# Kernel tuning notes

Hardware: AMD Instinct MI355X
Metric: run time of the kernel (lower is better)

## Reference

```python
import jax, jax.numpy as jnp
import numpy as np

EMBED_DIM = 1024
NUM_HEADS = 16
HEAD_DIM = EMBED_DIM // NUM_HEADS
B, T = 2, 2048


def setup_inputs() -> dict:
    key = jax.random.key(0)
    ks = jax.random.split(key, 5)
    s_in = 1.0 / np.sqrt(EMBED_DIM)
    return {
        "x": jax.random.normal(ks[0], (B, T, EMBED_DIM), dtype=jnp.float32),
        "qkv_w": jax.random.uniform(ks[1], (3 * EMBED_DIM, EMBED_DIM), jnp.float32, -s_in, s_in),
        "qkv_b": jax.random.uniform(ks[2], (3 * EMBED_DIM,), jnp.float32, -s_in, s_in),
        "out_w": jax.random.uniform(ks[3], (EMBED_DIM, EMBED_DIM), jnp.float32, -s_in, s_in),
        "out_b": jax.random.uniform(ks[4], (EMBED_DIM,), jnp.float32, -s_in, s_in),
    }


def reference(x, qkv_w, qkv_b, out_w, out_b):
    b, t, d = x.shape
    scale = HEAD_DIM ** -0.5
    # fused qkv projection: (B, T, 3D)
    qkv = jnp.einsum("btd,ed->bte", x, qkv_w) + qkv_b
    qkv = qkv.reshape(b, t, 3, NUM_HEADS, HEAD_DIM)
    q, k, v = jnp.moveaxis(qkv, 2, 0)  # each (B, T, H, Dh)
    # scores: (B, H, T, T)
    scores = jnp.einsum("bqhd,bkhd->bhqk", q, k) * scale
    attn = jax.nn.softmax(scores, axis=-1)
    # attention output: (B, T, H, Dh) -> (B, T, D)
    ctx = jnp.einsum("bhqk,bkhd->bqhd", attn, v).reshape(b, t, d)
    return jnp.einsum("btd,ed->bte", ctx, out_w) + out_b
```

## Files before the change

kernel.cpp:

```cpp
#include <hip/hip_runtime.h>

typedef __bf16 bf16;
typedef __bf16 bf16x4 __attribute__((ext_vector_type(4)));
typedef __bf16 bf16x8 __attribute__((ext_vector_type(8)));
typedef float f32x4 __attribute__((ext_vector_type(4)));

#define MFMA16(a, b, c) __builtin_amdgcn_mfma_f32_16x16x32_bf16(a, b, c, 0, 0, 0)

__device__ __forceinline__ void lds_load16(void* lds, const void* g) {
  __builtin_amdgcn_global_load_lds(
      (const __attribute__((address_space(1))) unsigned int*)g,
      (__attribute__((address_space(3))) unsigned int*)lds, 16, 0, 0);
}

__global__ void cvt3(const float* __restrict__ x, const float* __restrict__ qw,
                     const float* __restrict__ ow, bf16* __restrict__ xb,
                     bf16* __restrict__ qwb, bf16* __restrict__ owb) {
  const int i = blockIdx.x * blockDim.x + threadIdx.x;
  const float* src;
  bf16* dst;
  int k;
  if (i < 1048576) {
    src = x; dst = xb; k = i;
  } else if (i < 1048576 + 786432) {
    src = qw; dst = qwb; k = i - 1048576;
  } else {
    src = ow; dst = owb; k = i - (1048576 + 786432);
  }
  const float4 v = ((const float4*)src)[k];
  bf16x4 o;
  o[0] = (bf16)v.x; o[1] = (bf16)v.y; o[2] = (bf16)v.z; o[3] = (bf16)v.w;
  ((bf16x4*)dst)[k] = o;
}

__global__ __launch_bounds__(256, 2) void gemm_qkv(
    const bf16* __restrict__ A, const bf16* __restrict__ B,
    const float* __restrict__ bias, bf16* __restrict__ Qb,
    bf16* __restrict__ KF, bf16* __restrict__ VF) {
  const int K = 1024;
  __shared__ bf16 As[128][64];
  __shared__ bf16 Bs[128][64];
  const int tid = threadIdx.x;
  const int w = tid >> 6, lane = tid & 63;
  const int l15 = lane & 15, quad = lane >> 4;
  const int lr = lane >> 3;
  const int lc = (lane & 7) * 8;
  const int bn = blockIdx.x, bm = blockIdx.y;
  const int wm = (w >> 1) * 64, wn = (w & 1) * 64;

  const bf16* Abase = A + (size_t)(bm * 128) * K;
  const bf16* Bbase = B + (size_t)(bn * 128) * K;

  f32x4 acc[4][4] = {};

  for (int k0 = 0; k0 < K; k0 += 64) {
#pragma unroll
    for (int c = 0; c < 4; ++c) {
      const int row = w * 32 + c * 8;
      lds_load16(&As[row][0], Abase + (size_t)(row + lr) * K + k0 + lc);
      lds_load16(&Bs[row][0], Bbase + (size_t)(row + lr) * K + k0 + lc);
    }
    __syncthreads();
#pragma unroll
    for (int kk = 0; kk < 64; kk += 32) {
      bf16x8 am[4], bnf[4];
#pragma unroll
      for (int i = 0; i < 4; ++i)
        am[i] = *(const bf16x8*)&As[wm + i * 16 + l15][kk + quad * 8];
#pragma unroll
      for (int j = 0; j < 4; ++j)
        bnf[j] = *(const bf16x8*)&Bs[wn + j * 16 + l15][kk + quad * 8];
#pragma unroll
      for (int i = 0; i < 4; ++i)
#pragma unroll
        for (int j = 0; j < 4; ++j)
          acc[i][j] = MFMA16(am[i], bnf[j], acc[i][j]);
    }
    __syncthreads();
  }

#pragma unroll
  for (int j = 0; j < 4; ++j) {
    const int gcol = bn * 128 + wn + j * 16 + l15;
    const float bv = bias[gcol];
#pragma unroll
    for (int i = 0; i < 4; ++i) {
      const int t0 = bm * 128 + wm + i * 16 + quad * 4;
      if (gcol < 1024) {
#pragma unroll
        for (int r = 0; r < 4; ++r)
          Qb[(size_t)(t0 + r) * 1024 + gcol] =
              (bf16)((acc[i][j][r] + bv) * 0.18033688f);
      } else if (gcol < 2048) {
        const int dhl = gcol - 1024;
        const int hh = dhl >> 6, dh = dhl & 63;
        const int tl = t0 & 2047, bb = t0 >> 11;
        const size_t frag = ((size_t)(bb * 16 + hh) * 32 + (tl >> 6)) * 8 +
                            ((tl & 63) >> 4) * 2 + (dh >> 5);
        bf16* p = &KF[frag * 512 +
                      (size_t)(((dh >> 3) & 3) * 16 + (tl & 15)) * 8 + (dh & 7)];
#pragma unroll
        for (int r = 0; r < 4; ++r) p[r * 8] = (bf16)(acc[i][j][r] + bv);
      } else {
        const int dhl = gcol - 2048;
        const int hh = dhl >> 6, dh = dhl & 63;
        const int tl = t0 & 2047, bb = t0 >> 11;
        const size_t frag = ((size_t)(bb * 16 + hh) * 32 + (tl >> 6)) * 8 +
                            (dh >> 4) * 2 + ((tl & 63) >> 5);
        bf16x4 pv;
#pragma unroll
        for (int r = 0; r < 4; ++r) pv[r] = (bf16)(acc[i][j][r] + bv);
        *(bf16x4*)&VF[frag * 512 +
                      (size_t)(((tl & 31) >> 3) * 16 + (dh & 15)) * 8 +
                      (tl & 7)] = pv;
      }
    }
  }
}

__global__ __launch_bounds__(256, 2) void gemm_out(
    const bf16* __restrict__ A, const bf16* __restrict__ B,
    const float* __restrict__ bias, float* __restrict__ Cf) {
  __shared__ bf16 As[64][64];
  __shared__ bf16 Bs[128][64];
  const int tid = threadIdx.x;
  const int w = tid >> 6, lane = tid & 63;
  const int l15 = lane & 15, quad = lane >> 4;
  const int lr = lane >> 3, lc = (lane & 7) * 8;
  const int bn = blockIdx.x, bm = blockIdx.y;

  const bf16* Abase = A + (size_t)(bm * 64) * 1024;
  const bf16* Bbase = B + (size_t)(bn * 128) * 1024;

  f32x4 acc[4][2] = {};

  for (int k0 = 0; k0 < 1024; k0 += 64) {
#pragma unroll
    for (int c = 0; c < 2; ++c) {
      const int row = w * 16 + c * 8;
      lds_load16(&As[row][0], Abase + (size_t)(row + lr) * 1024 + k0 + lc);
    }
#pragma unroll
    for (int c = 0; c < 4; ++c) {
      const int row = w * 32 + c * 8;
      lds_load16(&Bs[row][0], Bbase + (size_t)(row + lr) * 1024 + k0 + lc);
    }
    __syncthreads();
#pragma unroll
    for (int kk = 0; kk < 64; kk += 32) {
      bf16x8 am[4], bnf[2];
#pragma unroll
      for (int i = 0; i < 4; ++i)
        am[i] = *(const bf16x8*)&As[i * 16 + l15][kk + quad * 8];
#pragma unroll
      for (int j = 0; j < 2; ++j)
        bnf[j] = *(const bf16x8*)&Bs[w * 32 + j * 16 + l15][kk + quad * 8];
#pragma unroll
      for (int i = 0; i < 4; ++i)
#pragma unroll
        for (int j = 0; j < 2; ++j)
          acc[i][j] = MFMA16(am[i], bnf[j], acc[i][j]);
    }
    __syncthreads();
  }

#pragma unroll
  for (int j = 0; j < 2; ++j) {
    const int gcol = bn * 128 + w * 32 + j * 16 + l15;
    const float bv = bias[gcol];
#pragma unroll
    for (int i = 0; i < 4; ++i)
#pragma unroll
      for (int r = 0; r < 4; ++r) {
        const int grow = bm * 64 + i * 16 + quad * 4 + r;
        Cf[(size_t)grow * 1024 + gcol] = acc[i][j][r] + bv;
      }
  }
}

__global__ __launch_bounds__(256, 2) void attn(const bf16* __restrict__ Qb,
                                               const bf16* __restrict__ KF,
                                               const bf16* __restrict__ VF,
                                               bf16* __restrict__ CTX) {
  __shared__ bf16 Ps[128][72];
  const int tid = threadIdx.x, w = tid >> 6, lane = tid & 63;
  const int l15 = lane & 15, quad = lane >> 4;
  const int blk = blockIdx.x;
  const int slot = blk & 7, grp = blk >> 3;
  const int qt = grp & 15, bh = (grp >> 4) * 8 + slot;
  const int h = bh & 15, b = bh >> 4;
  const int q0 = qt * 128;

  const bf16* qrow0 =
      Qb + (size_t)(b * 2048 + q0 + w * 32 + l15) * 1024 + h * 64;
  const bf16* qrow1 = qrow0 + (size_t)16 * 1024;
  const bf16x8 bq0a = *(const bf16x8*)&qrow0[quad * 8];
  const bf16x8 bq0b = *(const bf16x8*)&qrow0[32 + quad * 8];
  const bf16x8 bq1a = *(const bf16x8*)&qrow1[quad * 8];
  const bf16x8 bq1b = *(const bf16x8*)&qrow1[32 + quad * 8];

  const bf16* kfb = KF + (size_t)(b * 16 + h) * 131072 + (size_t)lane * 8;
  const bf16* vfb = VF + (size_t)(b * 16 + h) * 131072 + (size_t)lane * 8;

  bf16x8 kf[2][4], vf[2][4];
#pragma unroll
  for (int j = 0; j < 4; ++j)
#pragma unroll
    for (int k2 = 0; k2 < 2; ++k2) {
      kf[k2][j] = *(const bf16x8*)&kfb[(j * 2 + k2) << 9];
      vf[k2][j] = *(const bf16x8*)&vfb[(j * 2 + k2) << 9];
    }

  float l_run[2] = {0.f, 0.f};
  f32x4 o[2][4] = {};

  for (int kt6 = 0; kt6 < 32; ++kt6) {
    f32x4 s[2][4] = {};
#pragma unroll
    for (int k2 = 0; k2 < 2; ++k2)
#pragma unroll
      for (int j = 0; j < 4; ++j) {
        s[0][j] = MFMA16(kf[k2][j], k2 ? bq0b : bq0a, s[0][j]);
        s[1][j] = MFMA16(kf[k2][j], k2 ? bq1b : bq1a, s[1][j]);
      }

    {
      const bf16* kn = kfb + ((size_t)(kt6 + 1) << 12);
#pragma unroll
      for (int j = 0; j < 4; ++j)
#pragma unroll
        for (int k2 = 0; k2 < 2; ++k2)
          kf[k2][j] = *(const bf16x8*)&kn[(j * 2 + k2) << 9];
    }

#pragma unroll
    for (int i = 0; i < 2; ++i) {
      float sum = 0.f;
#pragma unroll
      for (int j = 0; j < 4; ++j) {
        bf16x4 pk;
#pragma unroll
        for (int r = 0; r < 4; ++r) {
          const float p = __builtin_amdgcn_exp2f(s[i][j][r]);
          sum += p;
          pk[r] = (bf16)p;
        }
        *(bf16x4*)&Ps[w * 32 + i * 16 + l15][j * 16 + quad * 4] = pk;
      }
      l_run[i] += sum;
    }

#pragma unroll
    for (int k2 = 0; k2 < 2; ++k2) {
      const bf16x8 bp0 = *(const bf16x8*)&Ps[w * 32 + l15][k2 * 32 + quad * 8];
      const bf16x8 bp1 =
          *(const bf16x8*)&Ps[w * 32 + 16 + l15][k2 * 32 + quad * 8];
#pragma unroll
      for (int j = 0; j < 4; ++j) {
        o[0][j] = MFMA16(vf[k2][j], bp0, o[0][j]);
        o[1][j] = MFMA16(vf[k2][j], bp1, o[1][j]);
      }
    }

    {
      const bf16* vn = vfb + ((size_t)(kt6 + 1) << 12);
#pragma unroll
      for (int j = 0; j < 4; ++j)
#pragma unroll
        for (int k2 = 0; k2 < 2; ++k2)
          vf[k2][j] = *(const bf16x8*)&vn[(j * 2 + k2) << 9];
    }
  }

#pragma unroll
  for (int i = 0; i < 2; ++i) {
    l_run[i] += __shfl_xor(l_run[i], 16);
    l_run[i] += __shfl_xor(l_run[i], 32);
  }

#pragma unroll
  for (int i = 0; i < 2; ++i) {
    const float inv = 1.f / l_run[i];
    bf16* crow =
        CTX + (size_t)(b * 2048 + q0 + w * 32 + i * 16 + l15) * 1024 + h * 64;
#pragma unroll
    for (int j = 0; j < 4; ++j) {
      bf16x4 ov;
#pragma unroll
      for (int r = 0; r < 4; ++r) ov[r] = (bf16)(o[i][j][r] * inv);
      *(bf16x4*)&crow[j * 16 + quad * 4] = ov;
    }
  }
}

extern "C" void kernel_launch(void* const* d_in, const int* in_sizes, int n_in,
                              void* d_out, int out_size, void* d_ws,
                              size_t ws_size, hipStream_t stream) {
  const float* x = (const float*)d_in[0];
  const float* qkv_w = (const float*)d_in[1];
  const float* qkv_b = (const float*)d_in[2];
  const float* out_w = (const float*)d_in[3];
  const float* out_b = (const float*)d_in[4];
  float* out = (float*)d_out;

  bf16* xb = (bf16*)d_ws;
  bf16* wqkv = xb + (size_t)4096 * 1024;
  bf16* wout = wqkv + (size_t)3072 * 1024;
  bf16* qb = wout + (size_t)1024 * 1024;
  bf16* kf = qb + (size_t)4096 * 1024;
  bf16* vf = kf + (size_t)4096 * 1024;
  bf16* ctx = vf + (size_t)4096 * 1024;

  cvt3<<<2097152 / 256, 256, 0, stream>>>(x, qkv_w, out_w, xb, wqkv, wout);

  gemm_qkv<<<dim3(24, 32), 256, 0, stream>>>(xb, wqkv, qkv_b, qb, kf, vf);
  attn<<<512, 256, 0, stream>>>(qb, kf, vf, ctx);
  gemm_out<<<dim3(8, 64), 256, 0, stream>>>(ctx, wout, out_b, out);
}
```

Measured before the change: 189.0 us.

## Stage K/V tiles in double-buffered LDS via global_load_lds shared across waves

Previously each of the four waves loaded the full K and V tiles from global memory into registers every iteration, so every block read each tile four times. Now the block cooperatively streams each 64-key K/V tile into a double-buffered LDS region with async global-to-LDS loads, prefetching the next tile while computing on the current one. Waves then read their MFMA operands from LDS. This cuts global/L2 traffic fourfold but adds a block-wide barrier per iteration and more LDS reads, and raises LDS use, which may affect occupancy.

```diff
diff --git a/kernel.cpp b/kernel.cpp
--- a/kernel.cpp
+++ b/kernel.cpp
@@ -182,6 +182,8 @@
                                                const bf16* __restrict__ KF,
                                                const bf16* __restrict__ VF,
                                                bf16* __restrict__ CTX) {
+  __shared__ bf16 Kb[2][4096];
+  __shared__ bf16 Vb[2][4096];
   __shared__ bf16 Ps[128][72];
   const int tid = threadIdx.x, w = tid >> 6, lane = tid & 63;
   const int l15 = lane & 15, quad = lane >> 4;
@@ -199,39 +201,43 @@
   const bf16x8 bq1a = *(const bf16x8*)&qrow1[quad * 8];
   const bf16x8 bq1b = *(const bf16x8*)&qrow1[32 + quad * 8];
 
-  const bf16* kfb = KF + (size_t)(b * 16 + h) * 131072 + (size_t)lane * 8;
-  const bf16* vfb = VF + (size_t)(b * 16 + h) * 131072 + (size_t)lane * 8;
-
-  bf16x8 kf[2][4], vf[2][4];
-#pragma unroll
-  for (int j = 0; j < 4; ++j)
-#pragma unroll
-    for (int k2 = 0; k2 < 2; ++k2) {
-      kf[k2][j] = *(const bf16x8*)&kfb[(j * 2 + k2) << 9];
-      vf[k2][j] = *(const bf16x8*)&vfb[(j * 2 + k2) << 9];
-    }
+  const bf16* kfs = KF + (size_t)(b * 16 + h) * 131072;
+  const bf16* vfs = VF + (size_t)(b * 16 + h) * 131072;
+  const int so = w * 1024;
+
+#pragma unroll
+  for (int c = 0; c < 2; ++c) {
+    lds_load16(&Kb[0][so + c * 512], kfs + so + c * 512 + lane * 8);
+    lds_load16(&Vb[0][so + c * 512], vfs + so + c * 512 + lane * 8);
+  }
 
   float l_run[2] = {0.f, 0.f};
   f32x4 o[2][4] = {};
 
   for (int kt6 = 0; kt6 < 32; ++kt6) {
+    const int cur = kt6 & 1;
+    const bf16* kcur = Kb[cur];
+    const bf16* vcur = Vb[cur];
+    __syncthreads();
+
+    if (kt6 < 31) {
+      const size_t nb = (size_t)(kt6 + 1) * 4096;
+#pragma unroll
+      for (int c = 0; c < 2; ++c) {
+        lds_load16(&Kb[cur ^ 1][so + c * 512], kfs + nb + so + c * 512 + lane * 8);
+        lds_load16(&Vb[cur ^ 1][so + c * 512], vfs + nb + so + c * 512 + lane * 8);
+      }
+    }
+
     f32x4 s[2][4] = {};
 #pragma unroll
     for (int k2 = 0; k2 < 2; ++k2)
 #pragma unroll
       for (int j = 0; j < 4; ++j) {
-        s[0][j] = MFMA16(kf[k2][j], k2 ? bq0b : bq0a, s[0][j]);
-        s[1][j] = MFMA16(kf[k2][j], k2 ? bq1b : bq1a, s[1][j]);
-      }
-
-    {
-      const bf16* kn = kfb + ((size_t)(kt6 + 1) << 12);
-#pragma unroll
-      for (int j = 0; j < 4; ++j)
-#pragma unroll
-        for (int k2 = 0; k2 < 2; ++k2)
-          kf[k2][j] = *(const bf16x8*)&kn[(j * 2 + k2) << 9];
-    }
+        const bf16x8 ak = *(const bf16x8*)&kcur[(j * 2 + k2) * 512 + lane * 8];
+        s[0][j] = MFMA16(ak, k2 ? bq0b : bq0a, s[0][j]);
+        s[1][j] = MFMA16(ak, k2 ? bq1b : bq1a, s[1][j]);
+      }
 
 #pragma unroll
     for (int i = 0; i < 2; ++i) {
@@ -257,18 +263,10 @@
           *(const bf16x8*)&Ps[w * 32 + 16 + l15][k2 * 32 + quad * 8];
 #pragma unroll
       for (int j = 0; j < 4; ++j) {
-        o[0][j] = MFMA16(vf[k2][j], bp0, o[0][j]);
-        o[1][j] = MFMA16(vf[k2][j], bp1, o[1][j]);
-      }
-    }
-
-    {
-      const bf16* vn = vfb + ((size_t)(kt6 + 1) << 12);
-#pragma unroll
-      for (int j = 0; j < 4; ++j)
-#pragma unroll
-        for (int k2 = 0; k2 < 2; ++k2)
-          vf[k2][j] = *(const bf16x8*)&vn[(j * 2 + k2) << 9];
+        const bf16x8 av = *(const bf16x8*)&vcur[(j * 2 + k2) * 512 + lane * 8];
+        o[0][j] = MFMA16(av, bp0, o[0][j]);
+        o[1][j] = MFMA16(av, bp1, o[1][j]);
+      }
     }
   }
 
```

Result: no change. 186.8 us (-1.2%).
